# Kernel tuning notes

Hardware: AMD Instinct MI355X
Metric: run time of the kernel (lower is better)

## Reference

```python
import jax, jax.numpy as jnp
import numpy as np

ENERGY_PERCENT = 0.8


def setup_inputs() -> dict:
    key = jax.random.key(0)
    B, T, C = 32, 4096, 128
    x = jax.random.normal(key, (B, T, C), dtype=jnp.float32)
    return {"x": x}


def reference(x):
    # x: [B, T, C]; FFT along time axis.
    T = x.shape[1]
    xf = jnp.fft.rfft(x, axis=1)                      # [B, F, C] complex
    energies = jnp.abs(xf) ** 2                       # [B, F, C]

    # Sort energies descending along freq axis (per batch, per channel).
    sorted_indices = jnp.argsort(-energies, axis=1)   # [B, F, C] int
    sorted_energies = jnp.take_along_axis(energies, sorted_indices, axis=1)

    total_energy = jnp.sum(energies, axis=1, keepdims=True)        # [B, 1, C]
    cumulative = jnp.cumsum(sorted_energies, axis=1)               # [B, F, C]

    # Smallest k such that cumulative energy exceeds energy_percent of total.
    exceeded = cumulative > total_energy * ENERGY_PERCENT          # [B, F, C] bool
    k = jnp.argmax(exceeded, axis=1) + 1                           # [B, C]

    # rank[b, f, c] = position of frequency f in the descending energy order;
    # this is the inverse permutation of sorted_indices (argsort of a permutation).
    rank = jnp.argsort(sorted_indices, axis=1)                     # [B, F, C]

    is_low_freq = rank < k[:, None, :]                             # [B, F, C]

    # Zero out the high-energy ("low-frequency") components -> residual x_var.
    mask = jnp.where(is_low_freq, 0.0, 1.0).astype(x.dtype)        # [B, F, C]
    x_var = jnp.fft.irfft(xf * mask, n=T, axis=1)                  # [B, T, C]
    x_inv = x - x_var
    return (x_var, x_inv)
```

## Files before the change

### kernel.cpp

```cpp
#include <hip/hip_runtime.h>


#define TLEN 4096
#define N2   2048
#define CCH  128
#define BB   32
#define HALF 16777216
#define PI_F 3.14159265358979323846f

#define LP(i) ((i) + ((i) >> 5))
#define ZLEN 2113

__device__ __forceinline__ void cmul(float& r, float& i, float br, float bi) {
  float tr = r * br - i * bi;
  i = r * bi + i * br;
  r = tr;
}

__device__ __forceinline__ void dft4(float vr[4], float vi[4], float s) {
  float t0r = vr[0] + vr[2], t0i = vi[0] + vi[2];
  float t1r = vr[0] - vr[2], t1i = vi[0] - vi[2];
  float t2r = vr[1] + vr[3], t2i = vi[1] + vi[3];
  float d3r = vr[1] - vr[3], d3i = vi[1] - vi[3];
  float t3r = -s * d3i, t3i = s * d3r;
  vr[0] = t0r + t2r; vi[0] = t0i + t2i;
  vr[1] = t1r + t3r; vi[1] = t1i + t3i;
  vr[2] = t0r - t2r; vi[2] = t0i - t2i;
  vr[3] = t1r - t3r; vi[3] = t1i - t3i;
}

__device__ __forceinline__ void dft8(float vr[8], float vi[8], float s) {
  float er[4]  = {vr[0], vr[2], vr[4], vr[6]};
  float ei[4]  = {vi[0], vi[2], vi[4], vi[6]};
  float odr[4] = {vr[1], vr[3], vr[5], vr[7]};
  float odi[4] = {vi[1], vi[3], vi[5], vi[7]};
  dft4(er, ei, s);
  dft4(odr, odi, s);
  const float c = 0.70710678118654752440f;
  float wr[4] = {1.0f, c, 0.0f, -c};
  float wi[4] = {0.0f, s * c, s, s * c};
  #pragma unroll
  for (int k = 0; k < 4; ++k) {
    float tr = wr[k] * odr[k] - wi[k] * odi[k];
    float ti = wr[k] * odi[k] + wi[k] * odr[k];
    vr[k]     = er[k] + tr; vi[k]     = ei[k] + ti;
    vr[k + 4] = er[k] - tr; vi[k + 4] = ei[k] - ti;
  }
}

__device__ __forceinline__ void stage8_first(float* zr, float* zi, int tid, float s) {
  float vr[8], vi[8];
  #pragma unroll
  for (int r = 0; r < 8; ++r) {
    int idx = LP(tid + (r << 8));
    vr[r] = zr[idx]; vi[r] = zi[idx];
  }
  dft8(vr, vi, s);
  __syncthreads();
  #pragma unroll
  for (int r = 0; r < 8; ++r) {
    int idx = LP((tid << 3) + r);
    zr[idx] = vr[r]; zi[idx] = vi[r];
  }
  __syncthreads();
}

template <int NS>
__device__ __forceinline__ void stage8_tw(float* zr, float* zi, int tid, float s) {
  int j = tid;
  int p = j & (NS - 1);
  float vr[8], vi[8];
  #pragma unroll
  for (int r = 0; r < 8; ++r) {
    int idx = LP(j + (r << 8));
    vr[r] = zr[idx]; vi[r] = zi[idx];
  }
  float ang = s * 6.28318530717958647692f * (float)p / (float)(NS * 8);
  float s1, c1; __sincosf(ang, &s1, &c1);
  float c2 = c1 * c1 - s1 * s1, s2 = 2.0f * c1 * s1;
  float c3 = c2 * c1 - s2 * s1, s3 = c2 * s1 + s2 * c1;
  float c4 = c2 * c2 - s2 * s2, s4 = 2.0f * c2 * s2;
  float c5 = c4 * c1 - s4 * s1, s5 = c4 * s1 + s4 * c1;
  float c6 = c4 * c2 - s4 * s2, s6 = c4 * s2 + s4 * c2;
  float c7 = c4 * c3 - s4 * s3, s7 = c4 * s3 + s4 * c3;
  cmul(vr[1], vi[1], c1, s1);
  cmul(vr[2], vi[2], c2, s2);
  cmul(vr[3], vi[3], c3, s3);
  cmul(vr[4], vi[4], c4, s4);
  cmul(vr[5], vi[5], c5, s5);
  cmul(vr[6], vi[6], c6, s6);
  cmul(vr[7], vi[7], c7, s7);
  dft8(vr, vi, s);
  __syncthreads();
  int idxD = ((j - p) << 3) + p;
  #pragma unroll
  for (int r = 0; r < 8; ++r) {
    int idx = LP(idxD + r * NS);
    zr[idx] = vr[r]; zi[idx] = vi[r];
  }
  __syncthreads();
}

__device__ __forceinline__ void stage4_last(float* zr, float* zi, int tid, float s) {
  #pragma unroll
  for (int half = 0; half < 2; ++half) {
    int j = tid + (half << 8);
    float ang = s * PI_F * (float)j * (1.0f / 1024.0f);
    float s1, c1; __sincosf(ang, &s1, &c1);
    float c2 = c1 * c1 - s1 * s1, s2 = 2.0f * c1 * s1;
    float c3 = c2 * c1 - s2 * s1, s3 = c2 * s1 + s2 * c1;
    float vr[4], vi[4];
    #pragma unroll
    for (int r = 0; r < 4; ++r) {
      int idx = LP(j + (r << 9));
      vr[r] = zr[idx]; vi[r] = zi[idx];
    }
    cmul(vr[1], vi[1], c1, s1);
    cmul(vr[2], vi[2], c2, s2);
    cmul(vr[3], vi[3], c3, s3);
    dft4(vr, vi, s);
    #pragma unroll
    for (int r = 0; r < 4; ++r) {
      int idx = LP(j + (r << 9));
      zr[idx] = vr[r]; zi[idx] = vi[r];
    }
  }
  __syncthreads();
}

__device__ __forceinline__ void fft2048(float* zr, float* zi, int tid, float s) {
  stage8_first(zr, zi, tid, s);
  stage8_tw<8>(zr, zi, tid, s);
  stage8_tw<64>(zr, zi, tid, s);
  stage4_last(zr, zi, tid, s);
}

__device__ __forceinline__ float group_sum(float v, float* redg, int tg, int bank) {
  #pragma unroll
  for (int o = 32; o > 0; o >>= 1) v += __shfl_down(v, o, 64);
  if ((tg & 63) == 0) redg[(bank << 2) + (tg >> 6)] = v;
  __syncthreads();
  int b4 = bank << 2;
  return redg[b4] + redg[b4 + 1] + redg[b4 + 2] + redg[b4 + 3];
}

__global__ __launch_bounds__(1024, 8) void fourier_filter_fused(const float* __restrict__ x,
                                                                float* __restrict__ xvar,
                                                                float* __restrict__ xinv) {
  __shared__ float z[2][4][ZLEN];
  __shared__ float red[64];

  int tidx = threadIdx.x;

  int bid = blockIdx.x;
  int r = bid & 7;
  int m = bid >> 3;
  int b = m >> 2;
  int ql = m & 3;
  int cg = (((r + b) & 7) << 2) | ql;
  int cbase = cg << 2;

  const float* xp = x + (size_t)b * (TLEN * CCH) + cbase;

  #pragma unroll
  for (int it = 0; it < 4; ++it) {
    int t = tidx + (it << 10);
    float4 v = *(const float4*)(xp + (size_t)t * CCH);
    float* dst = &z[t & 1][0][0];
    int k = LP(t >> 1);
    dst[k]            = v.x;
    dst[ZLEN + k]     = v.y;
    dst[2 * ZLEN + k] = v.z;
    dst[3 * ZLEN + k] = v.w;
  }
  __syncthreads();

  int g  = tidx >> 8;
  int tg = tidx & 255;
  float* Zr = z[0][g];
  float* Zi = z[1][g];
  float* redg = red + (g << 3);

  fft2048(Zr, Zi, tg, -1.0f);

  float eb[9];
  eb[8] = 0.0f;
  const float RC  = 0.92387953251128675613f;
  const float RSn = -0.38268343236508977173f;
  float ws, wc;
  __sincosf(-PI_F * (float)tg * (1.0f / 2048.0f), &ws, &wc);
  #pragma unroll
  for (int jj = 0; jj < 4; ++jj) {
    int k = tg + (jj << 8);
    int mkz = (N2 - k) & (N2 - 1);
    int ik = LP(k), im = LP(N2 - k);
    float akr = Zr[ik],      aki = Zi[ik];
    float bkr = Zr[LP(mkz)], bki = Zi[LP(mkz)];
    float Er  = 0.5f * (akr + bkr);
    float Ei  = 0.5f * (aki - bki);
    float Or_ = 0.5f * (aki + bki);
    float Oi  = 0.5f * (bkr - akr);
    float tr = wc * Or_ - ws * Oi;
    float ti = wc * Oi + ws * Or_;
    float x0r = Er + tr, x0i = Ei + ti;
    float x1r = Er - tr, x1i = ti - Ei;
    Zr[ik] = x0r; Zi[ik] = x0i;
    Zr[im] = x1r; Zi[im] = x1i;
    eb[2 * jj]     = x0r * x0r + x0i * x0i;
    eb[2 * jj + 1] = x1r * x1r + x1i * x1i;
    float nwc = wc * RC - ws * RSn;
    ws = wc * RSn + ws * RC; wc = nwc;
  }
  if (tg == 0) {
    int i4 = LP(1024);
    float re = Zr[i4], im_ = Zi[i4];
    Zi[i4] = -im_;
    eb[8] = re * re + im_ * im_;
  }

  float tloc = 0.0f;
  #pragma unroll
  for (int s = 0; s < 9; ++s) tloc += eb[s];
  float total = group_sum(tloc, redg, tg, 0);
  float thresh = 0.8f * total;

  unsigned lo = 0u, hi = 0x7F7FFFFFu;
  for (int it = 0; it < 31; ++it) {
    unsigned mid = (lo + hi + 1u) >> 1;
    float tau = __uint_as_float(mid);
    float loc = 0.0f;
    #pragma unroll
    for (int s = 0; s < 9; ++s) loc += (eb[s] >= tau) ? eb[s] : 0.0f;
    float ssum = group_sum(loc, redg, tg, (it + 1) & 1);
    if (ssum > thresh) lo = mid; else hi = mid - 1;
  }
  float tau = __uint_as_float(lo);

  const float RSp = 0.38268343236508977173f;
  __sincosf(PI_F * (float)tg * (1.0f / 2048.0f), &ws, &wc);
  #pragma unroll
  for (int jj = 0; jj < 4; ++jj) {
    int k = tg + (jj << 8);
    int ik = LP(k), im = LP(N2 - k);
    float xkr = Zr[ik], xki = Zi[ik];
    float xmr = Zr[im], xmi = Zi[im];
    float ekk = xkr * xkr + xki * xki;
    float emm = xmr * xmr + xmi * xmi;
    if (ekk >= tau) { xkr = 0.0f; xki = 0.0f; }
    if (emm >= tau) { xmr = 0.0f; xmi = 0.0f; }
    float Er = 0.5f * (xkr + xmr);
    float Ei = 0.5f * (xki - xmi);
    float Br = 0.5f * (xkr - xmr);
    float Bi = 0.5f * (xki + xmi);
    float Or_ = wc * Br - ws * Bi;
    float Oi  = wc * Bi + ws * Br;
    Zr[ik] = Er - Oi;  Zi[ik] = Ei + Or_;
    Zr[im] = Er + Oi;  Zi[im] = Or_ - Ei;
    float nwc = wc * RC - ws * RSp;
    ws = wc * RSp + ws * RC; wc = nwc;
  }
  if (tg == 0) {
    int i4 = LP(1024);
    float re = Zr[i4], im_ = Zi[i4];
    float e = re * re + im_ * im_;
    if (e >= tau) { re = 0.0f; im_ = 0.0f; }
    Zr[i4] = re; Zi[i4] = -im_;
  }
  __syncthreads();

  fft2048(Zr, Zi, tg, 1.0f);

  const float scale = 1.0f / 2048.0f;
  size_t base = (size_t)b * (TLEN * CCH) + cbase;
  #pragma unroll
  for (int it = 0; it < 4; ++it) {
    int t = tidx + (it << 10);
    const float* src = &z[t & 1][0][0];
    int k = LP(t >> 1);
    float4 v;
    v.x = src[k]            * scale;
    v.y = src[ZLEN + k]     * scale;
    v.z = src[2 * ZLEN + k] * scale;
    v.w = src[3 * ZLEN + k] * scale;
    size_t off = base + (size_t)t * CCH;
    float4 xv = *(const float4*)(x + off);
    *(float4*)(xvar + off) = v;
    *(float4*)(xinv + off) = make_float4(xv.x - v.x, xv.y - v.y, xv.z - v.z, xv.w - v.w);
  }
}

extern "C" void kernel_launch(void* const* d_in, const int* in_sizes, int n_in,
                              void* d_out, int out_size, void* d_ws, size_t ws_size,
                              hipStream_t stream) {
  const float* x = (const float*)d_in[0];
  float* out  = (float*)d_out;
  float* xvar = out;
  float* xinv = out + HALF;

  (void)d_ws; (void)ws_size;
  fourier_filter_fused<<<BB * 32, 1024, 0, stream>>>(x, xvar, xinv);
}
```

Before: 290.6 us.

## Replace 31-step threshold bisection with 4-pass radix histogram select; keep inputs in registers

Replaces the 31-iteration binary search over the float bit pattern, each step needing a block-wide reduction and barrier, with a 4-pass radix select. Each pass builds a 256-bin energy-sum histogram in shared memory using atomics, then runs a suffix scan to find the threshold digit. It also keeps the loaded input float4s in registers so the final x_inv computation no longer re-reads x from global memory. In exchange it adds shared-memory atomics, more registers per thread, and possible float-ordering differences in the histogram sums near the threshold.

Measured after the change: 349.5 us. +20.3%, slower.

```diff
diff --git a/kernel.cpp b/kernel.cpp
--- a/kernel.cpp
+++ b/kernel.cpp
@@ -135,20 +135,23 @@
   stage4_last(zr, zi, tid, s);
 }
 
-__device__ __forceinline__ float group_sum(float v, float* redg, int tg, int bank) {
+__device__ __forceinline__ float group_sum(float v, float* redg, int tg) {
   #pragma unroll
   for (int o = 32; o > 0; o >>= 1) v += __shfl_down(v, o, 64);
-  if ((tg & 63) == 0) redg[(bank << 2) + (tg >> 6)] = v;
-  __syncthreads();
-  int b4 = bank << 2;
-  return redg[b4] + redg[b4 + 1] + redg[b4 + 2] + redg[b4 + 3];
+  if ((tg & 63) == 0) redg[tg >> 6] = v;
+  __syncthreads();
+  return redg[0] + redg[1] + redg[2] + redg[3];
 }
 
 __global__ __launch_bounds__(1024, 8) void fourier_filter_fused(const float* __restrict__ x,
                                                                 float* __restrict__ xvar,
                                                                 float* __restrict__ xinv) {
   __shared__ float z[2][4][ZLEN];
-  __shared__ float red[64];
+  __shared__ float red[16];
+  __shared__ float hist[4][256];
+  __shared__ int   selD[4][8];
+  __shared__ float selS[4][8];
+  __shared__ float selB[4][8];
 
   int tidx = threadIdx.x;
 
@@ -162,24 +165,32 @@
 
   const float* xp = x + (size_t)b * (TLEN * CCH) + cbase;
 
+  float4 xr[4];
   #pragma unroll
   for (int it = 0; it < 4; ++it) {
     int t = tidx + (it << 10);
-    float4 v = *(const float4*)(xp + (size_t)t * CCH);
+    xr[it] = *(const float4*)(xp + (size_t)t * CCH);
+  }
+  hist[tidx >> 8][tidx & 255] = 0.0f;
+  #pragma unroll
+  for (int it = 0; it < 4; ++it) {
+    int t = tidx + (it << 10);
     float* dst = &z[t & 1][0][0];
     int k = LP(t >> 1);
-    dst[k]            = v.x;
-    dst[ZLEN + k]     = v.y;
-    dst[2 * ZLEN + k] = v.z;
-    dst[3 * ZLEN + k] = v.w;
+    dst[k]            = xr[it].x;
+    dst[ZLEN + k]     = xr[it].y;
+    dst[2 * ZLEN + k] = xr[it].z;
+    dst[3 * ZLEN + k] = xr[it].w;
   }
   __syncthreads();
 
   int g  = tidx >> 8;
   int tg = tidx & 255;
+  int lane = tg & 63;
+  int w = tg >> 6;
   float* Zr = z[0][g];
   float* Zi = z[1][g];
-  float* redg = red + (g << 3);
+  float* redg = red + (g << 2);
 
   fft2048(Zr, Zi, tg, -1.0f);
 
@@ -206,8 +217,12 @@
     float x1r = Er - tr, x1i = ti - Ei;
     Zr[ik] = x0r; Zi[ik] = x0i;
     Zr[im] = x1r; Zi[im] = x1i;
-    eb[2 * jj]     = x0r * x0r + x0i * x0i;
-    eb[2 * jj + 1] = x1r * x1r + x1i * x1i;
+    float e0 = x0r * x0r + x0i * x0i;
+    float e1 = x1r * x1r + x1i * x1i;
+    eb[2 * jj]     = e0;
+    eb[2 * jj + 1] = e1;
+    atomicAdd(&hist[g][__float_as_uint(e0) >> 24], e0);
+    atomicAdd(&hist[g][__float_as_uint(e1) >> 24], e1);
     float nwc = wc * RC - ws * RSn;
     ws = wc * RSn + ws * RC; wc = nwc;
   }
@@ -215,26 +230,64 @@
     int i4 = LP(1024);
     float re = Zr[i4], im_ = Zi[i4];
     Zi[i4] = -im_;
-    eb[8] = re * re + im_ * im_;
+    float e8 = re * re + im_ * im_;
+    eb[8] = e8;
+    atomicAdd(&hist[g][__float_as_uint(e8) >> 24], e8);
   }
 
   float tloc = 0.0f;
   #pragma unroll
   for (int s = 0; s < 9; ++s) tloc += eb[s];
-  float total = group_sum(tloc, redg, tg, 0);
+  float total = group_sum(tloc, redg, tg);
   float thresh = 0.8f * total;
 
-  unsigned lo = 0u, hi = 0x7F7FFFFFu;
-  for (int it = 0; it < 31; ++it) {
-    unsigned mid = (lo + hi + 1u) >> 1;
-    float tau = __uint_as_float(mid);
-    float loc = 0.0f;
+  unsigned prefix = 0u;
+  float s_above = 0.0f;
+  #pragma unroll
+  for (int pass = 0; pass < 4; ++pass) {
+    int shift = 24 - (pass << 3);
+    if (pass > 0) {
+      unsigned hm = 0xFFFFFFFFu << (shift + 8);
+      #pragma unroll
+      for (int s = 0; s < 9; ++s) {
+        unsigned bits = __float_as_uint(eb[s]);
+        if ((bits & hm) == prefix)
+          atomicAdd(&hist[g][(bits >> shift) & 255u], eb[s]);
+      }
+      __syncthreads();
+    }
+    float h = hist[g][tg];
+    hist[g][tg] = 0.0f;
+    float sfx = h;
     #pragma unroll
-    for (int s = 0; s < 9; ++s) loc += (eb[s] >= tau) ? eb[s] : 0.0f;
-    float ssum = group_sum(loc, redg, tg, (it + 1) & 1);
-    if (ssum > thresh) lo = mid; else hi = mid - 1;
-  }
-  float tau = __uint_as_float(lo);
+    for (int o = 1; o < 64; o <<= 1) {
+      float t2 = __shfl_down(sfx, o, 64);
+      sfx += (lane + o < 64) ? t2 : 0.0f;
+    }
+    if (lane == 0) selS[g][w] = sfx;
+    __syncthreads();
+    float addw = 0.0f;
+    #pragma unroll
+    for (int w2 = 1; w2 < 4; ++w2) addw += (w + w2 < 4) ? selS[g][w + w2] : 0.0f;
+    sfx += addw;
+    bool pred = (s_above + sfx > thresh);
+    unsigned long long mk = __ballot(pred);
+    if (mk != 0ull) {
+      if (lane == 63 - __clzll(mk)) { selD[g][w] = tg; selB[g][w] = sfx - h; }
+    } else if (lane == 0) {
+      selD[g][w] = -1;
+    }
+    __syncthreads();
+    int D = -1; float delta = 0.0f;
+    if (selD[g][3] >= 0)      { D = selD[g][3]; delta = selB[g][3]; }
+    else if (selD[g][2] >= 0) { D = selD[g][2]; delta = selB[g][2]; }
+    else if (selD[g][1] >= 0) { D = selD[g][1]; delta = selB[g][1]; }
+    else if (selD[g][0] >= 0) { D = selD[g][0]; delta = selB[g][0]; }
+    if (D < 0) { D = 0; delta = 0.0f; }
+    s_above += delta;
+    prefix |= ((unsigned)D) << shift;
+  }
+  float tau = __uint_as_float(prefix);
 
   const float RSp = 0.38268343236508977173f;
   __sincosf(PI_F * (float)tg * (1.0f / 2048.0f), &ws, &wc);
@@ -283,9 +336,9 @@
     v.z = src[2 * ZLEN + k] * scale;
     v.w = src[3 * ZLEN + k] * scale;
     size_t off = base + (size_t)t * CCH;
-    float4 xv = *(const float4*)(x + off);
     *(float4*)(xvar + off) = v;
-    *(float4*)(xinv + off) = make_float4(xv.x - v.x, xv.y - v.y, xv.z - v.z, xv.w - v.w);
+    *(float4*)(xinv + off) = make_float4(xr[it].x - v.x, xr[it].y - v.y,
+                                         xr[it].z - v.z, xr[it].w - v.w);
   }
 }
 
```
